# Kernel tuning notes

Measured on AMD Instinct MI355X. Metric: run time of the kernel, lower is better.

The kernel has to match this reference:

```python
import jax, jax.numpy as jnp
import numpy as np

ROOT = 512   # size of root group
FAN = 7      # children per root node
C = ROOT * (1 + FAN)  # 4096 total nodes
MAX_DEPTH = 8  # upper bound on parent-chain length (tree depth is 2 here)


def _build_tree():
    group_offsets = [0]
    group_sizes = [ROOT]
    cid_groups = [0] * ROOT
    parents = [-1] * ROOT
    off = ROOT
    for r in range(ROOT):
        group_offsets.append(off)
        group_sizes.append(FAN)
        cid_groups += [r + 1] * FAN
        parents += [r] * FAN
        off += FAN
    return (np.asarray(group_offsets, np.int32), np.asarray(group_sizes, np.int32),
            np.asarray(cid_groups, np.int32), np.asarray(parents, np.int32))


def setup_inputs() -> dict:
    key = jax.random.key(0)
    k1, k2 = jax.random.split(key)
    x = jax.random.normal(k1, (16, C, 26, 26), dtype=jnp.float32)
    label = jax.random.randint(k2, (16, 26, 26), 0, C, dtype=jnp.int32)
    go, gs, cg, pa = _build_tree()
    return {
        "x": x,
        "label": label,
        "group_offsets": jnp.asarray(go),
        "group_sizes": jnp.asarray(gs),
        "cid_groups": jnp.asarray(cg),
        "parents": jnp.asarray(pa),
    }


def reference(x, label, group_offsets, group_sizes, cid_groups, parents):
    # x: [N, C, H, W], label: [N, H, W] with node ids in [0, C)
    N, Cn, H, W = x.shape
    G = group_offsets.shape[0]
    M = N * H * W
    xT = x.transpose(1, 0, 2, 3).reshape(Cn, M)  # [C, M], positions ordered (N,H,W)
    # segmented (per-group) stable softmax over the node axis
    gmax = jax.ops.segment_max(xT, cid_groups, num_segments=G)        # [G, M]
    shifted = xT - gmax[cid_groups]                                   # [C, M]
    e = jnp.exp(shifted)
    gsum = jax.ops.segment_sum(e, cid_groups, num_segments=G)         # [G, M]
    logp = shifted - jnp.log(gsum)[cid_groups]                        # log prob, [C, M]
    # hierarchical loss: walk parent chain from the labeled node to the root
    lab = label.reshape(M)
    cols = jnp.arange(M)
    cur = lab
    loss = jnp.zeros((), x.dtype)
    for _ in range(MAX_DEPTH):
        valid = cur >= 0
        idx = jnp.clip(cur, 0, Cn - 1)
        lp = logp[idx, cols]
        loss = loss - jnp.sum(jnp.where(valid, lp, jnp.zeros((), x.dtype)))
        cur = jnp.where(valid, parents[idx], -1)
    # BATCH_SIZE normalization (valid_normalization=False): divide by outer num N
    norm = jnp.asarray(N, x.dtype)
    loss_weight = 1.0
    return loss / norm * loss_weight
```

## Files before the change

### kernel.cpp

```cpp
#include <hip/hip_runtime.h>
#include <hip/hip_bf16.h>

#define NIMG   16
#define CTOT   4096
#define HW     676
#define MTOT   (NIMG*HW)
#define ROOTN  512
#define NSLICE 4
#define CH_PER_SLICE (ROOTN/NSLICE)
#define CH_PER_WAVE  (CH_PER_SLICE/4)
#define PPB    64
#define NPB    (MTOT/PPB)
#define WS_BLK (NSLICE*MTOT)

__global__ __launch_bounds__(256) void tree_root_partial(
    const float* __restrict__ x, float* __restrict__ ws)
{
    __shared__ float red[4][64];
    const int lane = threadIdx.x & 63;
    const int wave = threadIdx.x >> 6;
    const int s    = blockIdx.x & 3;
    const int pb   = blockIdx.x >> 2;
    const int m    = pb * PPB + lane;
    const int n    = m / HW;
    const float* xb = x + (size_t)m + (size_t)n * (HW * (CTOT - 1));

    const int c0 = s * CH_PER_SLICE + wave * CH_PER_WAVE;
    float a0 = 0.f, a1 = 0.f, a2 = 0.f, a3 = 0.f;
    #pragma unroll
    for (int cc = 0; cc < CH_PER_WAVE; cc += 4) {
        float v0 = xb[(size_t)(c0 + cc + 0) * HW];
        float v1 = xb[(size_t)(c0 + cc + 1) * HW];
        float v2 = xb[(size_t)(c0 + cc + 2) * HW];
        float v3 = xb[(size_t)(c0 + cc + 3) * HW];
        a0 += __expf(v0);
        a1 += __expf(v1);
        a2 += __expf(v2);
        a3 += __expf(v3);
    }
    red[wave][lane] = (a0 + a1) + (a2 + a3);
    __syncthreads();
    if (wave == 0) {
        float r = (red[0][lane] + red[1][lane]) + (red[2][lane] + red[3][lane]);
        ws[s * MTOT + m] = r;
    }
}

__global__ __launch_bounds__(64) void tree_loss_pos(
    const float* __restrict__ x,
    const int*   __restrict__ label,
    const int*   __restrict__ group_offsets,
    const int*   __restrict__ group_sizes,
    const int*   __restrict__ cid_groups,
    const int*   __restrict__ parents,
    float*       __restrict__ ws)
{
    const int lane = threadIdx.x;
    const int m    = blockIdx.x * PPB + lane;
    const int n    = m / HW;
    const float* xb = x + (size_t)m + (size_t)n * (HW * (CTOT - 1));

    const float p0 = ws[0 * MTOT + m];
    const float p1 = ws[1 * MTOT + m];
    const float p2 = ws[2 * MTOT + m];
    const float p3 = ws[3 * MTOT + m];
    const int lab = label[m];
    const int g   = cid_groups[lab];

    float loss = 0.f;
    int troot = lab;
    if (g != 0) {
        const int off = group_offsets[g];
        const int sz  = group_sizes[g];
        float csum = 0.f, xlab = 0.f;
        for (int j = 0; j < sz; ++j) {
            float v = xb[(size_t)(off + j) * HW];
            csum += __expf(v);
            if (off + j == lab) xlab = v;
        }
        loss += xlab - __logf(csum);
        troot = parents[lab];
    }
    const float rsum = (p0 + p1) + (p2 + p3);
    loss += xb[(size_t)troot * HW] - __logf(rsum);

    #pragma unroll
    for (int d = 32; d > 0; d >>= 1)
        loss += __shfl_down(loss, d, 64);
    if (lane == 0) ws[WS_BLK + blockIdx.x] = loss;
}

__global__ __launch_bounds__(256) void tree_loss_final(
    const float* __restrict__ ws, float* __restrict__ out)
{
    __shared__ float sm[256];
    const int t = threadIdx.x;
    float v = 0.f;
    for (int i = t; i < NPB; i += 256) v += ws[WS_BLK + i];
    sm[t] = v;
    __syncthreads();
    #pragma unroll
    for (int s = 128; s > 0; s >>= 1) {
        if (t < s) sm[t] += sm[t + s];
        __syncthreads();
    }
    if (t == 0) out[0] = -sm[0] * (1.0f / (float)NIMG);
}

extern "C" void kernel_launch(void* const* d_in, const int* in_sizes, int n_in,
                              void* d_out, int out_size, void* d_ws, size_t ws_size,
                              hipStream_t stream)
{
    const float* x             = (const float*)d_in[0];
    const int*   label         = (const int*)d_in[1];
    const int*   group_offsets = (const int*)d_in[2];
    const int*   group_sizes   = (const int*)d_in[3];
    const int*   cid_groups    = (const int*)d_in[4];
    const int*   parents       = (const int*)d_in[5];
    float*       out           = (float*)d_out;
    float*       ws            = (float*)d_ws;

    tree_root_partial<<<NSLICE * NPB, 256, 0, stream>>>(x, ws);
    tree_loss_pos<<<NPB, 64, 0, stream>>>(x, label, group_offsets, group_sizes,
                                          cid_groups, parents, ws);
    tree_loss_final<<<1, 256, 0, stream>>>(ws, out);
}
```

Baseline: 225.6 us.

## Fuse root softmax and per-position loss into one kernel with hardcoded tree

```diff
diff --git a/kernel.cpp b/kernel.cpp
--- a/kernel.cpp
+++ b/kernel.cpp
@@ -1,127 +1,113 @@
 #include <hip/hip_runtime.h>
-#include <hip/hip_bf16.h>
 
 #define NIMG   16
 #define CTOT   4096
 #define HW     676
 #define MTOT   (NIMG*HW)
 #define ROOTN  512
-#define NSLICE 4
-#define CH_PER_SLICE (ROOTN/NSLICE)
-#define CH_PER_WAVE  (CH_PER_SLICE/4)
+#define FAN    7
 #define PPB    64
 #define NPB    (MTOT/PPB)
-#define WS_BLK (NSLICE*MTOT)
+#define WAVES  8
+#define CH_PER_WAVE (ROOTN/WAVES)
 
-__global__ __launch_bounds__(256) void tree_root_partial(
-    const float* __restrict__ x, float* __restrict__ ws)
+__global__ __launch_bounds__(512) void tree_fused(
+    const float* __restrict__ x,
+    const int*   __restrict__ label,
+    float*       __restrict__ ws)
 {
-    __shared__ float red[4][64];
-    const int lane = threadIdx.x & 63;
-    const int wave = threadIdx.x >> 6;
-    const int s    = blockIdx.x & 3;
-    const int pb   = blockIdx.x >> 2;
-    const int m    = pb * PPB + lane;
-    const int n    = m / HW;
-    const float* xb = x + (size_t)m + (size_t)n * (HW * (CTOT - 1));
+    __shared__ float red[WAVES][PPB];
+    __shared__ float wred[WAVES];
+    const int tid  = threadIdx.x;
+    const int lane = tid & 63;
+    const int wave = tid >> 6;
 
-    const int c0 = s * CH_PER_SLICE + wave * CH_PER_WAVE;
-    float a0 = 0.f, a1 = 0.f, a2 = 0.f, a3 = 0.f;
+    {
+        const int m = blockIdx.x * PPB + lane;
+        const int n = m / HW;
+        const float* xb = x + (size_t)m + (size_t)n * (size_t)(HW * (CTOT - 1));
+        const int c0 = wave * CH_PER_WAVE;
+        float a0 = 0.f, a1 = 0.f, a2 = 0.f, a3 = 0.f;
+        #pragma unroll
+        for (int cc = 0; cc < CH_PER_WAVE; cc += 4) {
+            float v0 = xb[(size_t)(c0 + cc + 0) * HW];
+            float v1 = xb[(size_t)(c0 + cc + 1) * HW];
+            float v2 = xb[(size_t)(c0 + cc + 2) * HW];
+            float v3 = xb[(size_t)(c0 + cc + 3) * HW];
+            a0 += __expf(v0);
+            a1 += __expf(v1);
+            a2 += __expf(v2);
+            a3 += __expf(v3);
+        }
+        red[wave][lane] = (a0 + a1) + (a2 + a3);
+    }
+    __syncthreads();
+
+    const int gid = tid >> 3;
+    const int sub = tid & 7;
+    const int m2  = blockIdx.x * PPB + gid;
+    const int n2  = m2 / HW;
+    const float* xc = x + (size_t)m2 + (size_t)n2 * (size_t)(HW * (CTOT - 1));
+    const int lab = label[m2];
+
+    float contrib = 0.f;
+    int troot = lab;
+    if (lab >= ROOTN) {
+        const int u   = lab - ROOTN;
+        const int r   = u / FAN;
+        const int off = ROOTN + r * FAN;
+        float e = 0.f, xl = 0.f;
+        if (sub < FAN) {
+            float v = xc[(size_t)(off + sub) * HW];
+            e  = __expf(v);
+            xl = (off + sub == lab) ? v : 0.f;
+        }
+        e += __shfl_xor(e, 4, 8);  xl += __shfl_xor(xl, 4, 8);
+        e += __shfl_xor(e, 2, 8);  xl += __shfl_xor(xl, 2, 8);
+        e += __shfl_xor(e, 1, 8);  xl += __shfl_xor(xl, 1, 8);
+        contrib = xl - __logf(e);
+        troot = r;
+    }
+
+    float tl = 0.f;
+    if (sub == 0) {
+        const float rs = ((red[0][gid] + red[1][gid]) + (red[2][gid] + red[3][gid]))
+                       + ((red[4][gid] + red[5][gid]) + (red[6][gid] + red[7][gid]));
+        tl = contrib + xc[(size_t)troot * HW] - __logf(rs);
+    }
+
     #pragma unroll
-    for (int cc = 0; cc < CH_PER_WAVE; cc += 4) {
-        float v0 = xb[(size_t)(c0 + cc + 0) * HW];
-        float v1 = xb[(size_t)(c0 + cc + 1) * HW];
-        float v2 = xb[(size_t)(c0 + cc + 2) * HW];
-        float v3 = xb[(size_t)(c0 + cc + 3) * HW];
-        a0 += __expf(v0);
-        a1 += __expf(v1);
-        a2 += __expf(v2);
-        a3 += __expf(v3);
-    }
-    red[wave][lane] = (a0 + a1) + (a2 + a3);
+    for (int d = 32; d > 0; d >>= 1) tl += __shfl_down(tl, d, 64);
+    if (lane == 0) wred[wave] = tl;
     __syncthreads();
-    if (wave == 0) {
-        float r = (red[0][lane] + red[1][lane]) + (red[2][lane] + red[3][lane]);
-        ws[s * MTOT + m] = r;
+    if (tid == 0) {
+        float s = 0.f;
+        #pragma unroll
+        for (int w = 0; w < WAVES; ++w) s += wred[w];
+        ws[blockIdx.x] = s;
     }
 }
 
-__global__ __launch_bounds__(64) void tree_loss_pos(
-    const float* __restrict__ x,
-    const int*   __restrict__ label,
-    const int*   __restrict__ group_offsets,
-    const int*   __restrict__ group_sizes,
-    const int*   __restrict__ cid_groups,
-    const int*   __restrict__ parents,
-    float*       __restrict__ ws)
-{
-    const int lane = threadIdx.x;
-    const int m    = blockIdx.x * PPB + lane;
-    const int n    = m / HW;
-    const float* xb = x + (size_t)m + (size_t)n * (HW * (CTOT - 1));
-
-    const float p0 = ws[0 * MTOT + m];
-    const float p1 = ws[1 * MTOT + m];
-    const float p2 = ws[2 * MTOT + m];
-    const float p3 = ws[3 * MTOT + m];
-    const int lab = label[m];
-    const int g   = cid_groups[lab];
-
-    float loss = 0.f;
-    int troot = lab;
-    if (g != 0) {
-        const int off = group_offsets[g];
-        const int sz  = group_sizes[g];
-        float csum = 0.f, xlab = 0.f;
-        for (int j = 0; j < sz; ++j) {
-            float v = xb[(size_t)(off + j) * HW];
-            csum += __expf(v);
-            if (off + j == lab) xlab = v;
-        }
-        loss += xlab - __logf(csum);
-        troot = parents[lab];
-    }
-    const float rsum = (p0 + p1) + (p2 + p3);
-    loss += xb[(size_t)troot * HW] - __logf(rsum);
-
-    #pragma unroll
-    for (int d = 32; d > 0; d >>= 1)
-        loss += __shfl_down(loss, d, 64);
-    if (lane == 0) ws[WS_BLK + blockIdx.x] = loss;
-}
-
-__global__ __launch_bounds__(256) void tree_loss_final(
+__global__ __launch_bounds__(64) void tree_final(
     const float* __restrict__ ws, float* __restrict__ out)
 {
-    __shared__ float sm[256];
     const int t = threadIdx.x;
     float v = 0.f;
-    for (int i = t; i < NPB; i += 256) v += ws[WS_BLK + i];
-    sm[t] = v;
-    __syncthreads();
+    for (int i = t; i < NPB; i += 64) v += ws[i];
     #pragma unroll
-    for (int s = 128; s > 0; s >>= 1) {
-        if (t < s) sm[t] += sm[t + s];
-        __syncthreads();
-    }
-    if (t == 0) out[0] = -sm[0] * (1.0f / (float)NIMG);
+    for (int d = 32; d > 0; d >>= 1) v += __shfl_down(v, d, 64);
+    if (t == 0) out[0] = -v * (1.0f / (float)NIMG);
 }
 
 extern "C" void kernel_launch(void* const* d_in, const int* in_sizes, int n_in,
                               void* d_out, int out_size, void* d_ws, size_t ws_size,
                               hipStream_t stream)
 {
-    const float* x             = (const float*)d_in[0];
-    const int*   label         = (const int*)d_in[1];
-    const int*   group_offsets = (const int*)d_in[2];
-    const int*   group_sizes   = (const int*)d_in[3];
-    const int*   cid_groups    = (const int*)d_in[4];
-    const int*   parents       = (const int*)d_in[5];
-    float*       out           = (float*)d_out;
-    float*       ws            = (float*)d_ws;
+    const float* x     = (const float*)d_in[0];
+    const int*   label = (const int*)d_in[1];
+    float* out = (float*)d_out;
+    float* ws  = (float*)d_ws;
 
-    tree_root_partial<<<NSLICE * NPB, 256, 0, stream>>>(x, ws);
-    tree_loss_pos<<<NPB, 64, 0, stream>>>(x, label, group_offsets, group_sizes,
-                                          cid_groups, parents, ws);
-    tree_loss_final<<<1, 256, 0, stream>>>(ws, out);
+    tree_fused<<<NPB, 512, 0, stream>>>(x, label, ws);
+    tree_final<<<1, 64, 0, stream>>>(ws, out);
 }
```

Measured after the change: 220.2 us. 1.02x faster.
